# Performance work log

Hardware: AMD Instinct MI355X
Metric: run time of the kernel (lower is better)

The kernel has to match this reference:

```python
import jax, jax.numpy as jnp
import numpy as np

B, T, D, H = 64, 200, 256, 512


def setup_inputs() -> dict:
    key = jax.random.key(0)
    k0, k1, k2, k3 = jax.random.split(key, 4)
    return {
        "input_": jax.random.normal(k0, (B, T, D), jnp.float32),
        "duration": jax.random.uniform(k1, (B, T), jnp.float32),  # positive elapsed times
        "Wx": jax.random.normal(k2, (D, 7 * H), jnp.float32) / np.float32(np.sqrt(D)),
        "Wh": jax.random.normal(k3, (H, 7 * H), jnp.float32) / np.float32(np.sqrt(H)),
        "b": jnp.zeros((7 * H,), jnp.float32),
    }


def reference(input_, duration, Wx, Wh, b):
    """Continuous-time LSTM (Neural Hawkes). Returns stacked states (4, B, T, H)
    in the order (c, cbar, delta, o), matching CTLSTM.forward's tuple output."""
    hid = Wh.shape[0]

    def cell(carry, xt_dt):
        c, cbar, delta, o = carry
        xt, dt = xt_dt  # xt: (B, D), dt: (B,)
        # get_ctlstm_hidden: decay cell toward cbar over elapsed time dt
        c_t = cbar + (c - cbar) * jnp.exp(-delta * dt[:, None])
        h_t = o * jnp.tanh(c_t)
        # 7 fused gates: i, f, z, o, ibar, fbar, delta
        g = xt @ Wx + h_t @ Wh + b  # (B, 7H)
        gi, gf, gz, go, gib, gfb, gd = jnp.split(g, 7, axis=-1)
        i = jax.nn.sigmoid(gi)
        f = jax.nn.sigmoid(gf)
        z = jnp.tanh(gz)
        o_new = jax.nn.sigmoid(go)
        ibar = jax.nn.sigmoid(gib)
        fbar = jax.nn.sigmoid(gfb)
        d_new = jax.nn.softplus(gd)
        c_new = f * c_t + i * z
        cbar_new = fbar * cbar + ibar * z
        st = (c_new, cbar_new, d_new, o_new)
        return st, st

    bsz = input_.shape[0]
    z0 = jnp.zeros((bsz, hid), input_.dtype)
    init = (z0, z0, z0, z0)  # init_hidden: all-zero (c, cbar, delta, o)
    xs = (jnp.swapaxes(input_, 0, 1), jnp.swapaxes(duration, 0, 1))  # time-major
    _, outs = jax.lax.scan(cell, init, xs)  # each: (T, B, H)
    return jnp.stack([jnp.swapaxes(a, 0, 1) for a in outs], axis=0)  # (4, B, T, H)
```

## Files before the change

### kernel.cpp

```cpp
#include <hip/hip_runtime.h>
#include <hip/hip_bf16.h>
#include <math.h>

#define BB 64
#define TT 200
#define DD 256
#define HH 512
#define NCOL 3584
#define NGRP 4
#define NBLK (NGRP * 32)

using bf16x8 = __attribute__((ext_vector_type(8))) short;
using f32x4  = __attribute__((ext_vector_type(4))) float;

__device__ __forceinline__ float frcp_(float x) { return __builtin_amdgcn_rcpf(x); }
__device__ __forceinline__ float sigmoidf_(float x) {
    return frcp_(1.0f + __expf(-x));
}
__device__ __forceinline__ float tanhf_(float x) {
    return 1.0f - 2.0f * frcp_(__expf(2.0f * x) + 1.0f);
}
__device__ __forceinline__ float softplusf_(float x) {
    return fmaxf(x, 0.0f) + __logf(1.0f + __expf(-fabsf(x)));
}
__device__ __forceinline__ short f2bf(float f) {
    union { float f; unsigned u; } v; v.f = f;
    unsigned r = v.u + 0x7fff + ((v.u >> 16) & 1);
    return (short)(r >> 16);
}
__device__ __forceinline__ float bf2f(short s) {
    union { unsigned u; float f; } v; v.u = ((unsigned)(unsigned short)s) << 16;
    return v.f;
}

__global__ __launch_bounds__(256) void convert_x_kernel(
    const float* __restrict__ in, short* __restrict__ Xbf)
{
    int idx = blockIdx.x * 256 + threadIdx.x;
    float4 v = ((const float4*)in)[idx];
    short4 s;
    s.x = f2bf(v.x); s.y = f2bf(v.y); s.z = f2bf(v.z); s.w = f2bf(v.w);
    ((short4*)Xbf)[idx] = s;
}

__global__ __launch_bounds__(256) void pack_wx_kernel(
    const float* __restrict__ Wx, short* __restrict__ WxP)
{
    int idx = blockIdx.x * 256 + threadIdx.x;
    int jj = idx & 7, lane = (idx >> 3) & 63, kt = (idx >> 9) & 7, nt = idx >> 12;
    int k = kt * 32 + ((lane >> 4) << 3) + jj;
    int col = nt * 16 + (lane & 15);
    WxP[idx] = f2bf(Wx[(size_t)k * NCOL + col]);
}

__global__ __launch_bounds__(256) void pack_wh_kernel(
    const float* __restrict__ Wh, short* __restrict__ WhP)
{
    int idx = blockIdx.x * 256 + threadIdx.x;
    int jj = idx & 7, lane = (idx >> 3) & 63, kt = (idx >> 9) & 15;
    int gj = idx >> 13;
    int g = gj % 7, j0 = gj / 7;
    int k = kt * 32 + ((lane >> 4) << 3) + jj;
    int col = g * HH + j0 * 16 + (lane & 15);
    WhP[idx] = f2bf(Wh[(size_t)k * NCOL + col]);
}

__global__ __launch_bounds__(256) void precompute_kernel(
    const short* __restrict__ Xbf, const short* __restrict__ WxP,
    const float* __restrict__ bias, short* __restrict__ Xb)
{
    const int tid = threadIdx.x;
    const int lane = tid & 63;
    const int w = tid >> 6;
    const int nb = blockIdx.x;
    const int mb = blockIdx.y;

    f32x4 acc[8];
    #pragma unroll
    for (int i = 0; i < 8; ++i) acc[i] = (f32x4){0.f, 0.f, 0.f, 0.f};

    const int rowA = mb * 64 + w * 16 + (lane & 15);
    const short* __restrict__ ha = Xbf + (size_t)rowA * DD + ((lane >> 4) << 3);
    const short* __restrict__ wbase = WxP + ((size_t)(nb * 8) * 512 + lane) * 8;

    #pragma unroll
    for (int kt = 0; kt < 8; ++kt) {
        bf16x8 a = *(const bf16x8*)(ha + kt * 32);
        #pragma unroll
        for (int i = 0; i < 8; ++i) {
            bf16x8 b = *(const bf16x8*)(wbase + i * 4096 + kt * 512);
            acc[i] = __builtin_amdgcn_mfma_f32_16x16x32_bf16(a, b, acc[i], 0, 0, 0);
        }
    }

    const int colL = lane & 15;
    const int rBase = mb * 64 + w * 16 + ((lane >> 4) << 2);
    #pragma unroll
    for (int i = 0; i < 8; ++i) {
        const int col = (nb * 8 + i) * 16 + colL;
        const float bv = bias[col];
        #pragma unroll
        for (int r = 0; r < 4; ++r) {
            Xb[(size_t)(rBase + r) * NCOL + col] = f2bf(acc[i][r] + bv);
        }
    }
}

__global__ __launch_bounds__(64, 1) void recurrent_kernel(
    const short* __restrict__ Xb,
    const short* __restrict__ WhP,
    const float* __restrict__ dur,
    unsigned long long* __restrict__ h0,
    unsigned long long* __restrict__ h1,
    unsigned* __restrict__ flags,
    float* __restrict__ out)
{
    __shared__ short whL[7 * 16 * 64 * 8];

    const int lane = threadIdx.x;
    const int grp = blockIdx.x >> 5;
    const int j0 = blockIdx.x & 31;

    {
        const bf16x8* __restrict__ src = (const bf16x8*)(WhP + (size_t)j0 * 57344);
        bf16x8* dst = (bf16x8*)whL;
        #pragma unroll
        for (int i = 0; i < 112; ++i) dst[i * 64 + lane] = src[i * 64 + lane];
    }
    __syncthreads();

    const int colL = lane & 15;
    const int b = grp * 16 + colL;
    const int hcolBase = j0 * 16 + ((lane >> 4) << 2);
    const int kOff = (lane >> 4) << 3;
    const size_t hB64base = ((size_t)b * HH + kOff) >> 2;
    const short* __restrict__ wlds = whL + lane * 8;
    const int myrep = j0 & 7;

    float cdecr[4] = {0.f, 0.f, 0.f, 0.f};
    float cbarr[4] = {0.f, 0.f, 0.f, 0.f};
    const size_t S = (size_t)BB * TT * HH;

    unsigned long long xq[7];
    {
        const unsigned long long* xb64 =
            (const unsigned long long*)(Xb + (size_t)b * TT * NCOL + hcolBase);
        #pragma unroll
        for (int g = 0; g < 7; ++g) xq[g] = xb64[g * (HH / 4)];
    }
    float dtn = dur[b * TT + 1];

    #pragma unroll 1
    for (int t = 0; t < TT; ++t) {
        unsigned long long hr[32];
        if (t > 0) {
            const unsigned* fl =
                flags + (((size_t)(t - 1) * NGRP + grp) * 8 + myrep) * 32;
            while (true) {
                unsigned f = (lane < 32)
                    ? __hip_atomic_load(fl + lane, __ATOMIC_RELAXED,
                                        __HIP_MEMORY_SCOPE_AGENT)
                    : 1u;
                if (__all((int)(f != 0))) break;
                __builtin_amdgcn_s_sleep(1);
            }
            const unsigned long long* hin = (t & 1) ? h1 : h0;
            #pragma unroll
            for (int kt = 0; kt < 16; ++kt) {
                hr[2 * kt]     = __hip_atomic_load(&hin[hB64base + kt * 8],
                                    __ATOMIC_RELAXED, __HIP_MEMORY_SCOPE_AGENT);
                hr[2 * kt + 1] = __hip_atomic_load(&hin[hB64base + kt * 8 + 1],
                                    __ATOMIC_RELAXED, __HIP_MEMORY_SCOPE_AGENT);
            }
        } else {
            #pragma unroll
            for (int i = 0; i < 32; ++i) hr[i] = 0ull;
        }

        f32x4 acc[7];
        #pragma unroll
        for (int g = 0; g < 7; ++g) acc[g] = (f32x4){0.f, 0.f, 0.f, 0.f};

        #pragma unroll
        for (int kt = 0; kt < 16; ++kt) {
            union { unsigned long long q[2]; bf16x8 v; } u;
            u.q[0] = hr[2 * kt]; u.q[1] = hr[2 * kt + 1];
            const short* wkt = wlds + kt * 512;
            #pragma unroll
            for (int g = 0; g < 7; ++g) {
                bf16x8 a = *(const bf16x8*)(wkt + g * 8192);
                acc[g] = __builtin_amdgcn_mfma_f32_16x16x32_bf16(a, u.v, acc[g], 0, 0, 0);
            }
        }

        unsigned long long xqn[7];
        float dtnn;
        {
            const int tn = (t + 1 < TT) ? t + 1 : t;
            const unsigned long long* xb64n =
                (const unsigned long long*)(Xb + ((size_t)b * TT + tn) * NCOL + hcolBase);
            #pragma unroll
            for (int g = 0; g < 7; ++g) xqn[g] = xb64n[g * (HH / 4)];
            const int tn1 = (tn + 1 < TT) ? tn + 1 : TT - 1;
            dtnn = dur[b * TT + tn1];
        }

        f32x4 oc, ocb, od, oo;
        unsigned long long hq = 0ull;
        #pragma unroll
        for (int r = 0; r < 4; ++r) {
            const float gi  = acc[0][r] + bf2f((short)(xq[0] >> (16 * r)));
            const float gf  = acc[1][r] + bf2f((short)(xq[1] >> (16 * r)));
            const float gz  = acc[2][r] + bf2f((short)(xq[2] >> (16 * r)));
            const float go  = acc[3][r] + bf2f((short)(xq[3] >> (16 * r)));
            const float gib = acc[4][r] + bf2f((short)(xq[4] >> (16 * r)));
            const float gfb = acc[5][r] + bf2f((short)(xq[5] >> (16 * r)));
            const float gd  = acc[6][r] + bf2f((short)(xq[6] >> (16 * r)));

            const float i_  = sigmoidf_(gi);
            const float f_  = sigmoidf_(gf);
            const float z_  = tanhf_(gz);
            const float o_  = sigmoidf_(go);
            const float ib_ = sigmoidf_(gib);
            const float fb_ = sigmoidf_(gfb);
            const float d_  = softplusf_(gd);

            const float c_new  = f_ * cdecr[r] + i_ * z_;
            const float cb_new = fb_ * cbarr[r] + ib_ * z_;

            oc[r] = c_new; ocb[r] = cb_new; od[r] = d_; oo[r] = o_;

            const float cdn = cb_new + (c_new - cb_new) * __expf(-d_ * dtn);
            const float hn = o_ * tanhf_(cdn);
            cdecr[r] = cdn;
            cbarr[r] = cb_new;
            hq |= ((unsigned long long)(unsigned short)f2bf(hn)) << (16 * r);
        }

        if (t + 1 < TT) {
            unsigned long long* hout = (t & 1) ? h0 : h1;
            __hip_atomic_store(&hout[((size_t)b * HH + hcolBase) >> 2], hq,
                               __ATOMIC_RELAXED, __HIP_MEMORY_SCOPE_AGENT);
            asm volatile("s_waitcnt vmcnt(0)" ::: "memory");
            if (lane < 8) {
                __hip_atomic_store(
                    &flags[(((size_t)t * NGRP + grp) * 8 + lane) * 32 + j0], 1u,
                    __ATOMIC_RELAXED, __HIP_MEMORY_SCOPE_AGENT);
            }
        }

        const size_t ob = ((size_t)b * TT + t) * HH + hcolBase;
        *(f32x4*)(out + ob)         = oc;
        *(f32x4*)(out + ob + S)     = ocb;
        *(f32x4*)(out + ob + 2 * S) = od;
        *(f32x4*)(out + ob + 3 * S) = oo;

        #pragma unroll
        for (int g = 0; g < 7; ++g) xq[g] = xqn[g];
        dtn = dtnn;
    }
}

extern "C" void kernel_launch(void* const* d_in, const int* in_sizes, int n_in,
                              void* d_out, int out_size, void* d_ws, size_t ws_size,
                              hipStream_t stream) {
    const float* input = (const float*)d_in[0];
    const float* dur   = (const float*)d_in[1];
    const float* Wx    = (const float*)d_in[2];
    const float* Wh    = (const float*)d_in[3];
    const float* bias  = (const float*)d_in[4];
    float* out = (float*)d_out;

    short* Xb  = (short*)d_ws;
    short* Xbf = Xb + (size_t)TT * BB * NCOL;
    short* WxP = Xbf + (size_t)BB * TT * DD;
    short* WhP = WxP + 224 * 8 * 64 * 8;
    short* h0s = WhP + 32 * 7 * 16 * 64 * 8;
    short* h1s = h0s + BB * HH;
    unsigned* flags = (unsigned*)(h1s + BB * HH);

    hipMemsetAsync(flags, 0, (size_t)TT * NGRP * 8 * 32 * sizeof(unsigned), stream);

    convert_x_kernel<<<3200, 256, 0, stream>>>(input, Xbf);
    pack_wx_kernel<<<3584, 256, 0, stream>>>(Wx, WxP);
    pack_wh_kernel<<<7168, 256, 0, stream>>>(Wh, WhP);

    precompute_kernel<<<dim3(28, 200), 256, 0, stream>>>(Xbf, WxP, bias, Xb);

    recurrent_kernel<<<NBLK, 64, 0, stream>>>(
        Xb, WhP, dur,
        (unsigned long long*)h0s, (unsigned long long*)h1s,
        flags, out);
}
```

Baseline: 851.8 us.

## Interleave two batch groups per block to hide cross-block sync latency

Each recurrent block now handles two 16-row batch groups (64 blocks instead of 128) and alternates between them. While one group waits on its flag poll and h load, the block does the other group's GEMM and gate math. Flag publication and output stores are deferred so they overlap the other group's wait. This trades half the parallelism (fewer CUs) and doubled serial work per block for hiding inter-block synchronization latency.

```diff
diff --git a/kernel.cpp b/kernel.cpp
--- a/kernel.cpp
+++ b/kernel.cpp
@@ -8,10 +8,11 @@
 #define HH 512
 #define NCOL 3584
 #define NGRP 4
-#define NBLK (NGRP * 32)
+#define NBLK 64
 
 using bf16x8 = __attribute__((ext_vector_type(8))) short;
 using f32x4  = __attribute__((ext_vector_type(4))) float;
+typedef unsigned long long u64;
 
 __device__ __forceinline__ float frcp_(float x) { return __builtin_amdgcn_rcpf(x); }
 __device__ __forceinline__ float sigmoidf_(float x) {
@@ -106,19 +107,89 @@
     }
 }
 
+__device__ __forceinline__ void poll32(const unsigned* fl, int lane) {
+    while (true) {
+        unsigned f = (lane < 32)
+            ? __hip_atomic_load(fl + lane, __ATOMIC_RELAXED,
+                                __HIP_MEMORY_SCOPE_AGENT)
+            : 1u;
+        if (__all((int)(f != 0))) break;
+        __builtin_amdgcn_s_sleep(1);
+    }
+}
+__device__ __forceinline__ void load_h32(const u64* hp, u64 (&hr)[32]) {
+    #pragma unroll
+    for (int kt = 0; kt < 16; ++kt) {
+        hr[2 * kt]     = __hip_atomic_load(hp + kt * 8, __ATOMIC_RELAXED,
+                                           __HIP_MEMORY_SCOPE_AGENT);
+        hr[2 * kt + 1] = __hip_atomic_load(hp + kt * 8 + 1, __ATOMIC_RELAXED,
+                                           __HIP_MEMORY_SCOPE_AGENT);
+    }
+}
+__device__ __forceinline__ void gemm112(const u64 (&hr)[32],
+    const short* wlds, f32x4 (&acc)[7]) {
+    #pragma unroll
+    for (int kt = 0; kt < 16; ++kt) {
+        union { u64 q[2]; bf16x8 v; } u;
+        u.q[0] = hr[2 * kt]; u.q[1] = hr[2 * kt + 1];
+        const short* wkt = wlds + kt * 512;
+        #pragma unroll
+        for (int g = 0; g < 7; ++g) {
+            bf16x8 a = *(const bf16x8*)(wkt + g * 8192);
+            acc[g] = __builtin_amdgcn_mfma_f32_16x16x32_bf16(a, u.v, acc[g], 0, 0, 0);
+        }
+    }
+}
+__device__ __forceinline__ void step_math(
+    const f32x4 (&acc)[7], const u64 (&xq)[7], float dtn,
+    float (&cdecr)[4], float (&cbarr)[4],
+    f32x4 &oc, f32x4 &ocb, f32x4 &od, f32x4 &oo, u64 &hq)
+{
+    hq = 0ull;
+    #pragma unroll
+    for (int r = 0; r < 4; ++r) {
+        const float gi  = acc[0][r] + bf2f((short)(xq[0] >> (16 * r)));
+        const float gf  = acc[1][r] + bf2f((short)(xq[1] >> (16 * r)));
+        const float gz  = acc[2][r] + bf2f((short)(xq[2] >> (16 * r)));
+        const float go  = acc[3][r] + bf2f((short)(xq[3] >> (16 * r)));
+        const float gib = acc[4][r] + bf2f((short)(xq[4] >> (16 * r)));
+        const float gfb = acc[5][r] + bf2f((short)(xq[5] >> (16 * r)));
+        const float gd  = acc[6][r] + bf2f((short)(xq[6] >> (16 * r)));
+
+        const float i_  = sigmoidf_(gi);
+        const float f_  = sigmoidf_(gf);
+        const float z_  = tanhf_(gz);
+        const float o_  = sigmoidf_(go);
+        const float ib_ = sigmoidf_(gib);
+        const float fb_ = sigmoidf_(gfb);
+        const float d_  = softplusf_(gd);
+
+        const float c_new  = f_ * cdecr[r] + i_ * z_;
+        const float cb_new = fb_ * cbarr[r] + ib_ * z_;
+
+        oc[r] = c_new; ocb[r] = cb_new; od[r] = d_; oo[r] = o_;
+
+        const float cdn = cb_new + (c_new - cb_new) * __expf(-d_ * dtn);
+        const float hn = o_ * tanhf_(cdn);
+        cdecr[r] = cdn;
+        cbarr[r] = cb_new;
+        hq |= ((u64)(unsigned short)f2bf(hn)) << (16 * r);
+    }
+}
+
 __global__ __launch_bounds__(64, 1) void recurrent_kernel(
     const short* __restrict__ Xb,
     const short* __restrict__ WhP,
     const float* __restrict__ dur,
-    unsigned long long* __restrict__ h0,
-    unsigned long long* __restrict__ h1,
+    u64* __restrict__ h0,
+    u64* __restrict__ h1,
     unsigned* __restrict__ flags,
     float* __restrict__ out)
 {
     __shared__ short whL[7 * 16 * 64 * 8];
 
     const int lane = threadIdx.x;
-    const int grp = blockIdx.x >> 5;
+    const int pair = blockIdx.x >> 5;
     const int j0 = blockIdx.x & 31;
 
     {
@@ -130,135 +201,135 @@
     __syncthreads();
 
     const int colL = lane & 15;
-    const int b = grp * 16 + colL;
+    const int gA = pair * 2, gB = pair * 2 + 1;
+    const int bA = gA * 16 + colL;
+    const int bB = gB * 16 + colL;
     const int hcolBase = j0 * 16 + ((lane >> 4) << 2);
     const int kOff = (lane >> 4) << 3;
-    const size_t hB64base = ((size_t)b * HH + kOff) >> 2;
+    const size_t hB64A = ((size_t)bA * HH + kOff) >> 2;
+    const size_t hB64B = ((size_t)bB * HH + kOff) >> 2;
     const short* __restrict__ wlds = whL + lane * 8;
     const int myrep = j0 & 7;
-
-    float cdecr[4] = {0.f, 0.f, 0.f, 0.f};
-    float cbarr[4] = {0.f, 0.f, 0.f, 0.f};
     const size_t S = (size_t)BB * TT * HH;
 
-    unsigned long long xq[7];
+    float cdecA[4] = {0.f, 0.f, 0.f, 0.f}, cbarA[4] = {0.f, 0.f, 0.f, 0.f};
+    float cdecB[4] = {0.f, 0.f, 0.f, 0.f}, cbarB[4] = {0.f, 0.f, 0.f, 0.f};
+
+    f32x4 dA_oc, dA_ocb, dA_od, dA_oo;  size_t dA_ob = 0;
+    f32x4 dB_oc, dB_ocb, dB_od, dB_oo;  size_t dB_ob = 0;
+
+    u64 xqA[7], xqB[7];
     {
-        const unsigned long long* xb64 =
-            (const unsigned long long*)(Xb + (size_t)b * TT * NCOL + hcolBase);
-        #pragma unroll
-        for (int g = 0; g < 7; ++g) xq[g] = xb64[g * (HH / 4)];
-    }
-    float dtn = dur[b * TT + 1];
+        const u64* xa = (const u64*)(Xb + (size_t)bA * TT * NCOL + hcolBase);
+        const u64* xb = (const u64*)(Xb + (size_t)bB * TT * NCOL + hcolBase);
+        #pragma unroll
+        for (int g = 0; g < 7; ++g) { xqA[g] = xa[g * (HH / 4)]; xqB[g] = xb[g * (HH / 4)]; }
+    }
+    float dtnA = dur[bA * TT + 1];
+    float dtnB = dur[bB * TT + 1];
 
     #pragma unroll 1
     for (int t = 0; t < TT; ++t) {
-        unsigned long long hr[32];
+        u64 hr[32];
+        f32x4 acc[7];
+
         if (t > 0) {
-            const unsigned* fl =
-                flags + (((size_t)(t - 1) * NGRP + grp) * 8 + myrep) * 32;
-            while (true) {
-                unsigned f = (lane < 32)
-                    ? __hip_atomic_load(fl + lane, __ATOMIC_RELAXED,
-                                        __HIP_MEMORY_SCOPE_AGENT)
-                    : 1u;
-                if (__all((int)(f != 0))) break;
-                __builtin_amdgcn_s_sleep(1);
+            poll32(flags + (((size_t)(t - 1) * NGRP + gA) * 8 + myrep) * 32, lane);
+            load_h32(((t & 1) ? h1 : h0) + hB64A, hr);
+            asm volatile("s_waitcnt vmcnt(0)" ::: "memory");
+            __builtin_amdgcn_sched_barrier(0);
+            if (lane < 8) {
+                __hip_atomic_store(
+                    &flags[(((size_t)(t - 1) * NGRP + gB) * 8 + lane) * 32 + j0], 1u,
+                    __ATOMIC_RELAXED, __HIP_MEMORY_SCOPE_AGENT);
             }
-            const unsigned long long* hin = (t & 1) ? h1 : h0;
-            #pragma unroll
-            for (int kt = 0; kt < 16; ++kt) {
-                hr[2 * kt]     = __hip_atomic_load(&hin[hB64base + kt * 8],
-                                    __ATOMIC_RELAXED, __HIP_MEMORY_SCOPE_AGENT);
-                hr[2 * kt + 1] = __hip_atomic_load(&hin[hB64base + kt * 8 + 1],
-                                    __ATOMIC_RELAXED, __HIP_MEMORY_SCOPE_AGENT);
-            }
+            *(f32x4*)(out + dB_ob)         = dB_oc;
+            *(f32x4*)(out + dB_ob + S)     = dB_ocb;
+            *(f32x4*)(out + dB_ob + 2 * S) = dB_od;
+            *(f32x4*)(out + dB_ob + 3 * S) = dB_oo;
         } else {
             #pragma unroll
             for (int i = 0; i < 32; ++i) hr[i] = 0ull;
         }
 
-        f32x4 acc[7];
-        #pragma unroll
-        for (int g = 0; g < 7; ++g) acc[g] = (f32x4){0.f, 0.f, 0.f, 0.f};
-
-        #pragma unroll
-        for (int kt = 0; kt < 16; ++kt) {
-            union { unsigned long long q[2]; bf16x8 v; } u;
-            u.q[0] = hr[2 * kt]; u.q[1] = hr[2 * kt + 1];
-            const short* wkt = wlds + kt * 512;
-            #pragma unroll
-            for (int g = 0; g < 7; ++g) {
-                bf16x8 a = *(const bf16x8*)(wkt + g * 8192);
-                acc[g] = __builtin_amdgcn_mfma_f32_16x16x32_bf16(a, u.v, acc[g], 0, 0, 0);
-            }
-        }
-
-        unsigned long long xqn[7];
-        float dtnn;
+        u64 xqnA[7]; float dtnnA;
         {
             const int tn = (t + 1 < TT) ? t + 1 : t;
-            const unsigned long long* xb64n =
-                (const unsigned long long*)(Xb + ((size_t)b * TT + tn) * NCOL + hcolBase);
+            const u64* xa = (const u64*)(Xb + ((size_t)bA * TT + tn) * NCOL + hcolBase);
             #pragma unroll
-            for (int g = 0; g < 7; ++g) xqn[g] = xb64n[g * (HH / 4)];
+            for (int g = 0; g < 7; ++g) xqnA[g] = xa[g * (HH / 4)];
             const int tn1 = (tn + 1 < TT) ? tn + 1 : TT - 1;
-            dtnn = dur[b * TT + tn1];
-        }
-
-        f32x4 oc, ocb, od, oo;
-        unsigned long long hq = 0ull;
-        #pragma unroll
-        for (int r = 0; r < 4; ++r) {
-            const float gi  = acc[0][r] + bf2f((short)(xq[0] >> (16 * r)));
-            const float gf  = acc[1][r] + bf2f((short)(xq[1] >> (16 * r)));
-            const float gz  = acc[2][r] + bf2f((short)(xq[2] >> (16 * r)));
-            const float go  = acc[3][r] + bf2f((short)(xq[3] >> (16 * r)));
-            const float gib = acc[4][r] + bf2f((short)(xq[4] >> (16 * r)));
-            const float gfb = acc[5][r] + bf2f((short)(xq[5] >> (16 * r)));
-            const float gd  = acc[6][r] + bf2f((short)(xq[6] >> (16 * r)));
-
-            const float i_  = sigmoidf_(gi);
-            const float f_  = sigmoidf_(gf);
-            const float z_  = tanhf_(gz);
-            const float o_  = sigmoidf_(go);
-            const float ib_ = sigmoidf_(gib);
-            const float fb_ = sigmoidf_(gfb);
-            const float d_  = softplusf_(gd);
-
-            const float c_new  = f_ * cdecr[r] + i_ * z_;
-            const float cb_new = fb_ * cbarr[r] + ib_ * z_;
-
-            oc[r] = c_new; ocb[r] = cb_new; od[r] = d_; oo[r] = o_;
-
-            const float cdn = cb_new + (c_new - cb_new) * __expf(-d_ * dtn);
-            const float hn = o_ * tanhf_(cdn);
-            cdecr[r] = cdn;
-            cbarr[r] = cb_new;
-            hq |= ((unsigned long long)(unsigned short)f2bf(hn)) << (16 * r);
-        }
+            dtnnA = dur[bA * TT + tn1];
+        }
+
+        #pragma unroll
+        for (int g = 0; g < 7; ++g) acc[g] = (f32x4){0.f, 0.f, 0.f, 0.f};
+        gemm112(hr, wlds, acc);
+
+        u64 hqA;
+        step_math(acc, xqA, dtnA, cdecA, cbarA, dA_oc, dA_ocb, dA_od, dA_oo, hqA);
+        dA_ob = ((size_t)bA * TT + t) * HH + hcolBase;
 
         if (t + 1 < TT) {
-            unsigned long long* hout = (t & 1) ? h0 : h1;
-            __hip_atomic_store(&hout[((size_t)b * HH + hcolBase) >> 2], hq,
+            u64* hout = (t & 1) ? h0 : h1;
+            __hip_atomic_store(&hout[((size_t)bA * HH + hcolBase) >> 2], hqA,
                                __ATOMIC_RELAXED, __HIP_MEMORY_SCOPE_AGENT);
-            asm volatile("s_waitcnt vmcnt(0)" ::: "memory");
-            if (lane < 8) {
-                __hip_atomic_store(
-                    &flags[(((size_t)t * NGRP + grp) * 8 + lane) * 32 + j0], 1u,
-                    __ATOMIC_RELAXED, __HIP_MEMORY_SCOPE_AGENT);
-            }
-        }
-
-        const size_t ob = ((size_t)b * TT + t) * HH + hcolBase;
-        *(f32x4*)(out + ob)         = oc;
-        *(f32x4*)(out + ob + S)     = ocb;
-        *(f32x4*)(out + ob + 2 * S) = od;
-        *(f32x4*)(out + ob + 3 * S) = oo;
-
-        #pragma unroll
-        for (int g = 0; g < 7; ++g) xq[g] = xqn[g];
-        dtn = dtnn;
-    }
+        }
+        #pragma unroll
+        for (int g = 0; g < 7; ++g) xqA[g] = xqnA[g];
+        dtnA = dtnnA;
+
+        if (t > 0) {
+            poll32(flags + (((size_t)(t - 1) * NGRP + gB) * 8 + myrep) * 32, lane);
+            load_h32(((t & 1) ? h1 : h0) + hB64B, hr);
+        } else {
+            #pragma unroll
+            for (int i = 0; i < 32; ++i) hr[i] = 0ull;
+        }
+        asm volatile("s_waitcnt vmcnt(0)" ::: "memory");
+        __builtin_amdgcn_sched_barrier(0);
+        if (t + 1 < TT && lane < 8) {
+            __hip_atomic_store(
+                &flags[(((size_t)t * NGRP + gA) * 8 + lane) * 32 + j0], 1u,
+                __ATOMIC_RELAXED, __HIP_MEMORY_SCOPE_AGENT);
+        }
+        *(f32x4*)(out + dA_ob)         = dA_oc;
+        *(f32x4*)(out + dA_ob + S)     = dA_ocb;
+        *(f32x4*)(out + dA_ob + 2 * S) = dA_od;
+        *(f32x4*)(out + dA_ob + 3 * S) = dA_oo;
+
+        u64 xqnB[7]; float dtnnB;
+        {
+            const int tn = (t + 1 < TT) ? t + 1 : t;
+            const u64* xb = (const u64*)(Xb + ((size_t)bB * TT + tn) * NCOL + hcolBase);
+            #pragma unroll
+            for (int g = 0; g < 7; ++g) xqnB[g] = xb[g * (HH / 4)];
+            const int tn1 = (tn + 1 < TT) ? tn + 1 : TT - 1;
+            dtnnB = dur[bB * TT + tn1];
+        }
+
+        #pragma unroll
+        for (int g = 0; g < 7; ++g) acc[g] = (f32x4){0.f, 0.f, 0.f, 0.f};
+        gemm112(hr, wlds, acc);
+
+        u64 hqB;
+        step_math(acc, xqB, dtnB, cdecB, cbarB, dB_oc, dB_ocb, dB_od, dB_oo, hqB);
+        dB_ob = ((size_t)bB * TT + t) * HH + hcolBase;
+
+        if (t + 1 < TT) {
+            u64* hout = (t & 1) ? h0 : h1;
+            __hip_atomic_store(&hout[((size_t)bB * HH + hcolBase) >> 2], hqB,
+                               __ATOMIC_RELAXED, __HIP_MEMORY_SCOPE_AGENT);
+        }
+        #pragma unroll
+        for (int g = 0; g < 7; ++g) xqB[g] = xqnB[g];
+        dtnB = dtnnB;
+    }
+
+    *(f32x4*)(out + dB_ob)         = dB_oc;
+    *(f32x4*)(out + dB_ob + S)     = dB_ocb;
+    *(f32x4*)(out + dB_ob + 2 * S) = dB_od;
+    *(f32x4*)(out + dB_ob + 3 * S) = dB_oo;
 }
 
 extern "C" void kernel_launch(void* const* d_in, const int* in_sizes, int n_in,
@@ -289,6 +360,6 @@
 
     recurrent_kernel<<<NBLK, 64, 0, stream>>>(
         Xb, WhP, dur,
-        (unsigned long long*)h0s, (unsigned long long*)h1s,
+        (u64*)h0s, (u64*)h1s,
         flags, out);
 }
```

Result: slower. 1.926 ms (+126.1%).
